# Kernel tuning notes

Hardware: AMD Instinct MI355X
Metric: run time of the kernel (lower is better)

The kernel has to match this reference:

```python
import jax, jax.numpy as jnp
import numpy as np

NB_POOLS = 115
EPS = 1e-12  # matches torch F.normalize default eps


def setup_inputs() -> dict:
    key = jax.random.key(0)
    x = jax.random.normal(key, (4, 256, 64, 64), dtype=jnp.float32)
    return {"x": x}


def reference(x):
    b, c, row, col = x.shape
    hw = row * col
    # L2 normalize over channel dim (torch F.normalize: x / max(||x||, eps))
    norm = jnp.sqrt(jnp.sum(x * x, axis=1, keepdims=True))
    xn = x / jnp.maximum(norm, EPS)
    xf = xn.reshape(b, c, hw)  # (b, c, HW)
    # self-correlation: corr[b, i, j] = sum_c xn[b,c,i] * xn[b,c,j] / c
    corr = jnp.einsum('bci,bcj->bij', xf, xf) / c  # (b, HW, HW)
    corr = corr.reshape(b, hw, row, col)           # (b, HW, row, col)
    # top-k over the source-pixel dim (dim=1): move it last for lax.top_k
    corr_t = jnp.moveaxis(corr, 1, -1)             # (b, row, col, HW)
    top_vals, _ = jax.lax.top_k(corr_t, NB_POOLS)  # (b, row, col, k)
    return jnp.moveaxis(top_vals, -1, 1)           # (b, k, row, col)
```

## Files before the change

kernel.cpp:

```cpp
#include <hip/hip_runtime.h>
#include <hip/hip_fp16.h>

#define CH 256
#define HW 4096
#define K_TOP 115
#define CAND 128
#define TPAD 152
#define NTRI 528
#define NTRI_H 264

typedef __attribute__((ext_vector_type(8))) short short8;
typedef __attribute__((ext_vector_type(4))) float f32x4;
typedef __attribute__((ext_vector_type(4))) unsigned int u32x4;

__device__ __forceinline__ unsigned short f32_to_bf16(float f) {
  union { float f; unsigned int u; } v; v.f = f;
  unsigned int r = v.u + 0x7fffu + ((v.u >> 16) & 1u);
  return (unsigned short)(r >> 16);
}

__device__ __forceinline__ unsigned int f16key(unsigned short h) {
  return (h & 0x8000u) ? (unsigned int)((unsigned short)~h)
                       : (unsigned int)(h | 0x8000u);
}

__device__ __forceinline__ unsigned short key2f16(unsigned int k) {
  return (k & 0x8000u) ? (unsigned short)(k ^ 0x8000u)
                       : (unsigned short)(~k & 0xffffu);
}

__global__ void norms_kernel(const float* __restrict__ x, float* __restrict__ rn) {
  int b = blockIdx.x >> 4;
  int p = ((blockIdx.x & 15) << 8) + threadIdx.x;
  const float* xb = x + (size_t)b * CH * HW + p;
  float ss = 0.f;
  #pragma unroll 8
  for (int c = 0; c < CH; ++c) { float v = xb[(size_t)c * HW]; ss += v * v; }
  rn[b * HW + p] = 1.0f / fmaxf(sqrtf(ss), 1e-12f);
}

__global__ void transpose_kernel(const float* __restrict__ x, const float* __restrict__ rn,
                                 unsigned short* __restrict__ xnT) {
  __shared__ float tile[64][65];
  int blk = blockIdx.x;
  int b = blk >> 8;
  int rem = blk & 255;
  int c0 = (rem >> 6) << 6;
  int p0 = (rem & 63) << 6;
  for (int idx = threadIdx.x; idx < 64 * 64; idx += blockDim.x) {
    int c = idx >> 6, p = idx & 63;
    tile[c][p] = x[((size_t)b * CH + c0 + c) * HW + p0 + p];
  }
  __syncthreads();
  for (int E = threadIdx.x; E < 512; E += blockDim.x) {
    int lr  = E & 15;
    int lk  = (E >> 4) & 3;
    int kkl = (E >> 6) & 1;
    int pgl = E >> 7;
    int pl = pgl * 16 + lr;
    int cl = kkl * 32 + lk * 8;
    float s = rn[b * HW + p0 + pl];
    unsigned int w0, w1, w2, w3;
    w0 = (unsigned int)f32_to_bf16(tile[cl + 0][pl] * s) |
         ((unsigned int)f32_to_bf16(tile[cl + 1][pl] * s) << 16);
    w1 = (unsigned int)f32_to_bf16(tile[cl + 2][pl] * s) |
         ((unsigned int)f32_to_bf16(tile[cl + 3][pl] * s) << 16);
    w2 = (unsigned int)f32_to_bf16(tile[cl + 4][pl] * s) |
         ((unsigned int)f32_to_bf16(tile[cl + 5][pl] * s) << 16);
    w3 = (unsigned int)f32_to_bf16(tile[cl + 6][pl] * s) |
         ((unsigned int)f32_to_bf16(tile[cl + 7][pl] * s) << 16);
    u32x4 w = {w0, w1, w2, w3};
    int pg  = (p0 >> 4) + pgl;
    int kkg = (c0 >> 5) + kkl;
    *(u32x4*)(xnT + ((((size_t)b * 256 + pg) * 8 + kkg) * 64 + lk * 16 + lr) * 8) = w;
  }
}

__launch_bounds__(256, 4)
__global__ void gram_kernel(const unsigned short* __restrict__ xnT,
                            unsigned short* __restrict__ gkeys, int nb) {
  __shared__ unsigned short tile[128 * TPAD];
  const int tid  = threadIdx.x;
  const int lane = tid & 63, wv = tid >> 6;
  const int wj = wv >> 1, wi = wv & 1;
  const int lr = lane & 15, lk = lane >> 4;

  int bb, t;
  if (nb == 4) {
    const int xcd = blockIdx.x & 7;
    bb = xcd >> 1;
    t  = ((xcd & 1) ? NTRI_H : 0) + (blockIdx.x >> 3);
  } else {
    bb = 0;
    t  = blockIdx.x;
  }
  int it = (int)((sqrtf(8.0f * (float)t + 1.0f) - 1.0f) * 0.5f);
  while (((it + 1) * (it + 2)) / 2 <= t) ++it;
  while ((it * (it + 1)) / 2 > t) --it;
  const int jt = t - (it * (it + 1)) / 2;
  const int j0 = jt * 128, i0 = it * 128;

  const short8* x8 = (const short8*)(xnT + (size_t)bb * HW * CH);
  unsigned short* gk = gkeys + (size_t)bb * HW * HW;

  f32x4 acc[4][4];
  #pragma unroll
  for (int m = 0; m < 4; ++m)
    #pragma unroll
    for (int n = 0; n < 4; ++n) acc[m][n] = (f32x4){0.f, 0.f, 0.f, 0.f};

  const int pgj = jt * 8 + wj * 4;
  const int pgi = it * 8 + wi * 4;
  #pragma unroll
  for (int kk = 0; kk < 8; ++kk) {
    short8 af[4], bf[4];
    #pragma unroll
    for (int m = 0; m < 4; ++m)
      af[m] = x8[(size_t)((pgj + m) * 8 + kk) * 64 + lane];
    #pragma unroll
    for (int n = 0; n < 4; ++n)
      bf[n] = x8[(size_t)((pgi + n) * 8 + kk) * 64 + lane];
    #pragma unroll
    for (int m = 0; m < 4; ++m)
      #pragma unroll
      for (int n = 0; n < 4; ++n)
        acc[m][n] = __builtin_amdgcn_mfma_f32_16x16x32_bf16(af[m], bf[n],
                                                            acc[m][n], 0, 0, 0);
  }

  #pragma unroll
  for (int m = 0; m < 4; ++m) {
    #pragma unroll
    for (int n = 0; n < 4; ++n) {
      #pragma unroll
      for (int r = 0; r < 4; ++r) {
        int jloc = wj * 64 + m * 16 + lk * 4 + r;
        int iloc = wi * 64 + n * 16 + lr;
        tile[jloc * TPAD + iloc] =
            (unsigned short)f16key(__half_as_ushort(__float2half(acc[m][n][r])));
      }
    }
  }
  __syncthreads();

  #pragma unroll
  for (int itr = 0; itr < 8; ++itr) {
    int idx = itr * 256 + tid;
    int row = idx >> 4, ch = idx & 15;
    u32x4 v = *(const u32x4*)&tile[row * TPAD + ch * 8];
    *(u32x4*)(gk + (size_t)(j0 + row) * HW + i0 + ch * 8) = v;
  }

  if (it != jt) {
    __syncthreads();
    #pragma unroll
    for (int m = 0; m < 4; ++m) {
      #pragma unroll
      for (int n = 0; n < 4; ++n) {
        int il  = wi * 64 + n * 16 + lr;
        int jl0 = wj * 64 + m * 16 + lk * 4;
        unsigned long long pk =
            (unsigned long long)f16key(__half_as_ushort(__float2half(acc[m][n][0]))) |
            ((unsigned long long)f16key(__half_as_ushort(__float2half(acc[m][n][1]))) << 16) |
            ((unsigned long long)f16key(__half_as_ushort(__float2half(acc[m][n][2]))) << 32) |
            ((unsigned long long)f16key(__half_as_ushort(__float2half(acc[m][n][3]))) << 48);
        *(unsigned long long*)&tile[il * TPAD + jl0] = pk;
      }
    }
    __syncthreads();

    #pragma unroll
    for (int itr = 0; itr < 8; ++itr) {
      int idx = itr * 256 + tid;
      int row = idx >> 4, ch = idx & 15;
      u32x4 v = *(const u32x4*)&tile[row * TPAD + ch * 8];
      *(u32x4*)(gk + (size_t)(i0 + row) * HW + j0 + ch * 8) = v;
    }
  }
}

__launch_bounds__(256, 4)
__global__ void select_kernel(const unsigned short* __restrict__ gkeys,
                              float* __restrict__ out, int b_base, int nb) {
  __shared__ __align__(16) unsigned short cand[4][CAND];
  __shared__ unsigned int rcnt[4][CAND];
  __shared__ unsigned int cnt[4];
  const int tid  = threadIdx.x;
  const int lane = tid & 63, wv = tid >> 6;
  int bb, cg;
  if (nb == 4) {
    const int xcd = blockIdx.x & 7;
    bb = xcd >> 1;
    cg = ((xcd & 1) << 9) + (blockIdx.x >> 3);
  } else {
    bb = 0;
    cg = blockIdx.x;
  }
  const int b = b_base + bb;
  const int j = cg * 4 + wv;

  const u32x4* cp4 = (const u32x4*)(gkeys + (size_t)bb * HW * HW + (size_t)j * HW);
  u32x4 q0 = cp4[0 * 64 + lane], q1 = cp4[1 * 64 + lane];
  u32x4 q2 = cp4[2 * 64 + lane], q3 = cp4[3 * 64 + lane];
  u32x4 q4 = cp4[4 * 64 + lane], q5 = cp4[5 * 64 + lane];
  u32x4 q6 = cp4[6 * 64 + lane], q7 = cp4[7 * 64 + lane];

  q0 = (q0 - 0x40004000u) | 0x80008000u;
  q1 = (q1 - 0x40004000u) | 0x80008000u;
  q2 = (q2 - 0x40004000u) | 0x80008000u;
  q3 = (q3 - 0x40004000u) | 0x80008000u;
  q4 = (q4 - 0x40004000u) | 0x80008000u;
  q5 = (q5 - 0x40004000u) | 0x80008000u;
  q6 = (q6 - 0x40004000u) | 0x80008000u;
  q7 = (q7 - 0x40004000u) | 0x80008000u;

  unsigned int lo = 0;
  #pragma unroll 1
  for (int bit = 14; bit >= 0; --bit) {
    const unsigned int m  = lo | (1u << bit);
    const unsigned int mm = m * 0x10001u;
    int c = 0;
    #define CNTV(Q) \
      c += (int)__builtin_popcount((Q.x - mm) & 0x80008000u); \
      c += (int)__builtin_popcount((Q.y - mm) & 0x80008000u); \
      c += (int)__builtin_popcount((Q.z - mm) & 0x80008000u); \
      c += (int)__builtin_popcount((Q.w - mm) & 0x80008000u);
    CNTV(q0) CNTV(q1) CNTV(q2) CNTV(q3)
    CNTV(q4) CNTV(q5) CNTV(q6) CNTV(q7)
    #undef CNTV
    c += __shfl_xor(c, 1);
    c += __shfl_xor(c, 2);
    c += __shfl_xor(c, 4);
    c += __shfl_xor(c, 8);
    c += __shfl_xor(c, 16);
    c += __shfl_xor(c, 32);
    if (c >= K_TOP) lo = m;
  }

  cand[wv][2 * lane]     = (unsigned short)lo;
  cand[wv][2 * lane + 1] = (unsigned short)lo;
  rcnt[wv][2 * lane]     = 0;
  rcnt[wv][2 * lane + 1] = 0;
  if (lane == 0) cnt[wv] = 0;

  #define GATH(v)                                                \
    { unsigned int _v = (v);                                     \
      if (_v > lo) {                                             \
        unsigned int _p = atomicAdd(&cnt[wv], 1u);               \
        cand[wv][_p] = (unsigned short)_v;                       \
      } }
  #define GATH4(Q)                                               \
    GATH(Q.x & 0x7fffu) GATH((Q.x >> 16) & 0x7fffu)              \
    GATH(Q.y & 0x7fffu) GATH((Q.y >> 16) & 0x7fffu)              \
    GATH(Q.z & 0x7fffu) GATH((Q.z >> 16) & 0x7fffu)              \
    GATH(Q.w & 0x7fffu) GATH((Q.w >> 16) & 0x7fffu)
  GATH4(q0) GATH4(q1) GATH4(q2) GATH4(q3)
  GATH4(q4) GATH4(q5) GATH4(q6) GATH4(q7)
  #undef GATH4
  #undef GATH

  __syncthreads();

  unsigned int k0 = cand[wv][2 * lane];
  unsigned int k1 = cand[wv][2 * lane + 1];
  const unsigned int t0 = (k0 + 1u) * 0x10001u;
  const unsigned int t1 = (k1 + 1u) * 0x10001u;
  int g0 = 0, g1 = 0;
  {
    const u32x4* cv = (const u32x4*)&cand[wv][0];
    #pragma unroll
    for (int r = 0; r < 16; ++r) {
      u32x4 p = cv[r];
      #define GCNT(W) { unsigned int Pt = (W) | 0x80008000u;                 \
        g0 += (int)__builtin_popcount((Pt - t0) & 0x80008000u);              \
        g1 += (int)__builtin_popcount((Pt - t1) & 0x80008000u); }
      GCNT(p.x) GCNT(p.y) GCNT(p.z) GCNT(p.w)
      #undef GCNT
    }
  }
  unsigned int o0 = atomicAdd(&rcnt[wv][g0], 1u);
  unsigned int o1 = atomicAdd(&rcnt[wv][g1], 1u);
  int r0 = g0 + (int)o0;
  int r1 = g1 + (int)o1;

  if (r0 < K_TOP)
    out[((size_t)b * K_TOP + r0) * HW + j] =
        __half2float(__ushort_as_half(key2f16(k0 + 0x4000u))) * (1.0f / 256.0f);
  if (r1 < K_TOP)
    out[((size_t)b * K_TOP + r1) * HW + j] =
        __half2float(__ushort_as_half(key2f16(k1 + 0x4000u))) * (1.0f / 256.0f);
}

extern "C" void kernel_launch(void* const* d_in, const int* in_sizes, int n_in,
                              void* d_out, int out_size, void* d_ws, size_t ws_size,
                              hipStream_t stream) {
  (void)in_sizes; (void)n_in; (void)out_size;
  const float* x = (const float*)d_in[0];
  float* out = (float*)d_out;
  float* rn = (float*)d_ws;
  unsigned short* xnT = (unsigned short*)((char*)d_ws + 65536);
  const size_t GK_OFF = 65536 + (size_t)8 * 1024 * 1024;
  const size_t ONE    = (size_t)HW * HW * 2;
  const size_t NEED_1 = GK_OFF + ONE;
  const size_t NEED_4 = GK_OFF + 4 * ONE;

  norms_kernel<<<64, 256, 0, stream>>>(x, rn);
  transpose_kernel<<<1024, 256, 0, stream>>>(x, rn, xnT);

  if (ws_size >= NEED_4) {
    unsigned short* gkeys = (unsigned short*)((char*)d_ws + GK_OFF);
    gram_kernel<<<4 * NTRI, 256, 0, stream>>>(xnT, gkeys, 4);
    select_kernel<<<4096, 256, 0, stream>>>(gkeys, out, 0, 4);
  } else if (ws_size >= NEED_1) {
    unsigned short* gkeys = (unsigned short*)((char*)d_ws + GK_OFF);
    for (int b = 0; b < 4; ++b) {
      gram_kernel<<<NTRI, 256, 0, stream>>>(xnT + (size_t)b * HW * CH, gkeys, 1);
      select_kernel<<<1024, 256, 0, stream>>>(gkeys, out, b, 1);
    }
  }
}
```

Before: 135.8 us.

## Pipeline gram and select across batches with double-buffered mixed kernel

Replaces the all-batches gram pass followed by an all-batches select pass with a software pipeline. A combined kernel computes the gram tiles for batch b+1 while running top-k selection for batch b, using two ping-ponged key buffers and a shared-memory union. The goal is to overlap the compute-bound MFMA work with the memory-bound selection and to shrink the working set from four gram matrices to two, which may fit better in cache. In exchange there are more kernel launches, serialization points between stages, and the loss of the per-XCD batch mapping used before.

Measured after the change: 170.7 us. 1.26x slower.

```diff
diff --git a/kernel.cpp b/kernel.cpp
--- a/kernel.cpp
+++ b/kernel.cpp
@@ -7,7 +7,6 @@
 #define CAND 128
 #define TPAD 152
 #define NTRI 528
-#define NTRI_H 264
 
 typedef __attribute__((ext_vector_type(8))) short short8;
 typedef __attribute__((ext_vector_type(4))) float f32x4;
@@ -76,32 +75,30 @@
   }
 }
 
-__launch_bounds__(256, 4)
-__global__ void gram_kernel(const unsigned short* __restrict__ xnT,
-                            unsigned short* __restrict__ gkeys, int nb) {
-  __shared__ unsigned short tile[128 * TPAD];
-  const int tid  = threadIdx.x;
+struct SelS {
+  unsigned short cand[4][CAND];
+  unsigned int   rcnt[4][CAND];
+  unsigned int   cnt[4];
+};
+union MixS {
+  unsigned short tile[128 * TPAD];
+  SelS sel;
+};
+
+__device__ __forceinline__ void gram_body(unsigned short* tile,
+                                          const unsigned short* __restrict__ xnTb,
+                                          unsigned short* __restrict__ gk,
+                                          int t, int tid) {
   const int lane = tid & 63, wv = tid >> 6;
   const int wj = wv >> 1, wi = wv & 1;
   const int lr = lane & 15, lk = lane >> 4;
 
-  int bb, t;
-  if (nb == 4) {
-    const int xcd = blockIdx.x & 7;
-    bb = xcd >> 1;
-    t  = ((xcd & 1) ? NTRI_H : 0) + (blockIdx.x >> 3);
-  } else {
-    bb = 0;
-    t  = blockIdx.x;
-  }
   int it = (int)((sqrtf(8.0f * (float)t + 1.0f) - 1.0f) * 0.5f);
   while (((it + 1) * (it + 2)) / 2 <= t) ++it;
   while ((it * (it + 1)) / 2 > t) --it;
   const int jt = t - (it * (it + 1)) / 2;
   const int j0 = jt * 128, i0 = it * 128;
-
-  const short8* x8 = (const short8*)(xnT + (size_t)bb * HW * CH);
-  unsigned short* gk = gkeys + (size_t)bb * HW * HW;
+  const short8* x8 = (const short8*)xnTb;
 
   f32x4 acc[4][4];
   #pragma unroll
@@ -179,27 +176,14 @@
   }
 }
 
-__launch_bounds__(256, 4)
-__global__ void select_kernel(const unsigned short* __restrict__ gkeys,
-                              float* __restrict__ out, int b_base, int nb) {
-  __shared__ __align__(16) unsigned short cand[4][CAND];
-  __shared__ unsigned int rcnt[4][CAND];
-  __shared__ unsigned int cnt[4];
-  const int tid  = threadIdx.x;
+__device__ __forceinline__ void select_body(SelS* s,
+                                            const unsigned short* __restrict__ gkb,
+                                            float* __restrict__ out,
+                                            int b, int cg, int tid) {
   const int lane = tid & 63, wv = tid >> 6;
-  int bb, cg;
-  if (nb == 4) {
-    const int xcd = blockIdx.x & 7;
-    bb = xcd >> 1;
-    cg = ((xcd & 1) << 9) + (blockIdx.x >> 3);
-  } else {
-    bb = 0;
-    cg = blockIdx.x;
-  }
-  const int b = b_base + bb;
   const int j = cg * 4 + wv;
 
-  const u32x4* cp4 = (const u32x4*)(gkeys + (size_t)bb * HW * HW + (size_t)j * HW);
+  const u32x4* cp4 = (const u32x4*)(gkb + (size_t)j * HW);
   u32x4 q0 = cp4[0 * 64 + lane], q1 = cp4[1 * 64 + lane];
   u32x4 q2 = cp4[2 * 64 + lane], q3 = cp4[3 * 64 + lane];
   u32x4 q4 = cp4[4 * 64 + lane], q5 = cp4[5 * 64 + lane];
@@ -237,17 +221,17 @@
     if (c >= K_TOP) lo = m;
   }
 
-  cand[wv][2 * lane]     = (unsigned short)lo;
-  cand[wv][2 * lane + 1] = (unsigned short)lo;
-  rcnt[wv][2 * lane]     = 0;
-  rcnt[wv][2 * lane + 1] = 0;
-  if (lane == 0) cnt[wv] = 0;
+  s->cand[wv][2 * lane]     = (unsigned short)lo;
+  s->cand[wv][2 * lane + 1] = (unsigned short)lo;
+  s->rcnt[wv][2 * lane]     = 0;
+  s->rcnt[wv][2 * lane + 1] = 0;
+  if (lane == 0) s->cnt[wv] = 0;
 
   #define GATH(v)                                                \
     { unsigned int _v = (v);                                     \
       if (_v > lo) {                                             \
-        unsigned int _p = atomicAdd(&cnt[wv], 1u);               \
-        cand[wv][_p] = (unsigned short)_v;                       \
+        unsigned int _p = atomicAdd(&s->cnt[wv], 1u);            \
+        s->cand[wv][_p] = (unsigned short)_v;                    \
       } }
   #define GATH4(Q)                                               \
     GATH(Q.x & 0x7fffu) GATH((Q.x >> 16) & 0x7fffu)              \
@@ -261,13 +245,13 @@
 
   __syncthreads();
 
-  unsigned int k0 = cand[wv][2 * lane];
-  unsigned int k1 = cand[wv][2 * lane + 1];
+  unsigned int k0 = s->cand[wv][2 * lane];
+  unsigned int k1 = s->cand[wv][2 * lane + 1];
   const unsigned int t0 = (k0 + 1u) * 0x10001u;
   const unsigned int t1 = (k1 + 1u) * 0x10001u;
   int g0 = 0, g1 = 0;
   {
-    const u32x4* cv = (const u32x4*)&cand[wv][0];
+    const u32x4* cv = (const u32x4*)&s->cand[wv][0];
     #pragma unroll
     for (int r = 0; r < 16; ++r) {
       u32x4 p = cv[r];
@@ -278,8 +262,8 @@
       #undef GCNT
     }
   }
-  unsigned int o0 = atomicAdd(&rcnt[wv][g0], 1u);
-  unsigned int o1 = atomicAdd(&rcnt[wv][g1], 1u);
+  unsigned int o0 = atomicAdd(&s->rcnt[wv][g0], 1u);
+  unsigned int o1 = atomicAdd(&s->rcnt[wv][g1], 1u);
   int r0 = g0 + (int)o0;
   int r1 = g1 + (int)o1;
 
@@ -289,6 +273,37 @@
   if (r1 < K_TOP)
     out[((size_t)b * K_TOP + r1) * HW + j] =
         __half2float(__ushort_as_half(key2f16(k1 + 0x4000u))) * (1.0f / 256.0f);
+}
+
+__launch_bounds__(256, 4)
+__global__ void gram_kernel(const unsigned short* __restrict__ xnTb,
+                            unsigned short* __restrict__ gk) {
+  __shared__ __align__(16) MixS ms;
+  gram_body(ms.tile, xnTb, gk, blockIdx.x, threadIdx.x);
+}
+
+__launch_bounds__(256, 4)
+__global__ void select_kernel(const unsigned short* __restrict__ gkb,
+                              float* __restrict__ out, int b) {
+  __shared__ __align__(16) SelS ss;
+  select_body(&ss, gkb, out, b, blockIdx.x, threadIdx.x);
+}
+
+__launch_bounds__(256, 4)
+__global__ void mix_kernel(const unsigned short* __restrict__ xnT,
+                           unsigned short* __restrict__ gk_g,
+                           const unsigned short* __restrict__ gk_s,
+                           float* __restrict__ out, int bg, int bs) {
+  __shared__ __align__(16) MixS ms;
+  const int blk = blockIdx.x;
+  const int r3 = blk % 3;
+  if (r3 == 0) {
+    gram_body(ms.tile, xnT + (size_t)bg * HW * CH, gk_g, blk / 3, threadIdx.x);
+  } else {
+    int sidx = (blk / 3) * 2 + r3 - 1;
+    if (sidx < 1024)
+      select_body(&ms.sel, gk_s, out, bs, sidx, threadIdx.x);
+  }
 }
 
 extern "C" void kernel_launch(void* const* d_in, const int* in_sizes, int n_in,
@@ -299,23 +314,27 @@
   float* out = (float*)d_out;
   float* rn = (float*)d_ws;
   unsigned short* xnT = (unsigned short*)((char*)d_ws + 65536);
-  const size_t GK_OFF = 65536 + (size_t)8 * 1024 * 1024;
-  const size_t ONE    = (size_t)HW * HW * 2;
-  const size_t NEED_1 = GK_OFF + ONE;
-  const size_t NEED_4 = GK_OFF + 4 * ONE;
+  const size_t GK_OFF   = 65536 + (size_t)8 * 1024 * 1024;
+  const size_t ONE      = (size_t)HW * HW * 2;
+  const size_t NEED_SEQ = GK_OFF + ONE;
+  const size_t NEED_PIPE = GK_OFF + 2 * ONE;
 
   norms_kernel<<<64, 256, 0, stream>>>(x, rn);
   transpose_kernel<<<1024, 256, 0, stream>>>(x, rn, xnT);
 
-  if (ws_size >= NEED_4) {
-    unsigned short* gkeys = (unsigned short*)((char*)d_ws + GK_OFF);
-    gram_kernel<<<4 * NTRI, 256, 0, stream>>>(xnT, gkeys, 4);
-    select_kernel<<<4096, 256, 0, stream>>>(gkeys, out, 0, 4);
-  } else if (ws_size >= NEED_1) {
-    unsigned short* gkeys = (unsigned short*)((char*)d_ws + GK_OFF);
+  if (ws_size >= NEED_PIPE) {
+    unsigned short* gk0 = (unsigned short*)((char*)d_ws + GK_OFF);
+    unsigned short* gk1 = gk0 + (size_t)HW * HW;
+    gram_kernel<<<NTRI, 256, 0, stream>>>(xnT, gk0);
+    mix_kernel<<<3 * NTRI, 256, 0, stream>>>(xnT, gk1, gk0, out, 1, 0);
+    mix_kernel<<<3 * NTRI, 256, 0, stream>>>(xnT, gk0, gk1, out, 2, 1);
+    mix_kernel<<<3 * NTRI, 256, 0, stream>>>(xnT, gk1, gk0, out, 3, 2);
+    select_kernel<<<1024, 256, 0, stream>>>(gk1, out, 3);
+  } else if (ws_size >= NEED_SEQ) {
+    unsigned short* gk0 = (unsigned short*)((char*)d_ws + GK_OFF);
     for (int b = 0; b < 4; ++b) {
-      gram_kernel<<<NTRI, 256, 0, stream>>>(xnT + (size_t)b * HW * CH, gkeys, 1);
-      select_kernel<<<1024, 256, 0, stream>>>(gkeys, out, b, 1);
-    }
-  }
-}
+      gram_kernel<<<NTRI, 256, 0, stream>>>(xnT + (size_t)b * HW * CH, gk0);
+      select_kernel<<<1024, 256, 0, stream>>>(gk0, out, b);
+    }
+  }
+}
```
